# Kernel tuning notes

Hardware: AMD Instinct MI355X
Metric: run time of the kernel (lower is better)

The kernel has to match this reference:

```python
import jax, jax.numpy as jnp
import numpy as np

B, S, H, NH, HD, V = 2, 2048, 1024, 16, 64, 32000
BASE = 10000.0
NEG = jnp.finfo(jnp.float32).min


def setup_inputs() -> dict:
    key = jax.random.key(0)
    ks = jax.random.split(key, 12)
    batch = jax.random.randint(ks[0], (B, S), 0, V)
    positions = jnp.broadcast_to(jnp.arange(S), (B, S))
    lengths = jax.random.randint(ks[1], (B,), 1, S + 1)  # >=1 to avoid fully-masked rows
    sc = 1.0 / np.sqrt(H)
    emb = jax.random.normal(ks[2], (V, H), dtype=jnp.float32) * 0.02
    wq = jax.random.normal(ks[3], (H, NH * HD), dtype=jnp.float32) * sc
    bq = jnp.zeros((NH * HD,), jnp.float32)
    wk = jax.random.normal(ks[4], (H, NH * HD), dtype=jnp.float32) * sc
    bk = jnp.zeros((NH * HD,), jnp.float32)
    wv = jax.random.normal(ks[5], (H, NH * HD), dtype=jnp.float32) * sc
    bv = jnp.zeros((NH * HD,), jnp.float32)
    wo = jax.random.normal(ks[6], (NH * HD, H), dtype=jnp.float32) * sc
    bo = jnp.zeros((H,), jnp.float32)
    return dict(batch=batch, positions=positions, lengths=lengths, emb=emb,
                wq=wq, bq=bq, wk=wk, bk=bk, wv=wv, bv=bv, wo=wo, bo=bo)


def _rope(x, positions):
    # x: [B, NH, S, HD]; positions: [B, S] int
    inv_freq = 1.0 / (BASE ** (jnp.arange(0, HD, 2, dtype=jnp.float32) / HD))  # [HD/2]
    freqs = positions.astype(jnp.float32)[..., None] * inv_freq               # [B, S, HD/2]
    ang = jnp.concatenate([freqs, freqs], axis=-1)                            # [B, S, HD]
    cos = jnp.cos(ang)[:, None]                                               # [B, 1, S, HD]
    sin = jnp.sin(ang)[:, None]
    x1, x2 = x[..., :HD // 2], x[..., HD // 2:]
    rot = jnp.concatenate([-x2, x1], axis=-1)
    return x * cos + rot * sin


def reference(batch, positions, lengths, emb, wq, bq, wk, bk, wv, bv, wo, bo):
    h = emb[batch]                                                 # [B, S, H]
    q = (h @ wq + bq).reshape(B, S, NH, HD).transpose(0, 2, 1, 3)  # [B, NH, S, HD]
    k = (h @ wk + bk).reshape(B, S, NH, HD).transpose(0, 2, 1, 3)
    v = (h @ wv + bv).reshape(B, S, NH, HD).transpose(0, 2, 1, 3)
    q = _rope(q, positions)
    k = _rope(k, positions)
    scores = jnp.einsum('bhqd,bhkd->bhqk', q, k) / np.sqrt(HD)     # [B, NH, S, S]
    causal = jnp.triu(jnp.full((S, S), NEG, jnp.float32), 1)
    pad = jnp.where(jnp.arange(S)[None, :] < lengths[:, None], 0.0, NEG)  # [B, S]
    mask = pad[:, None, None, :] + causal[None, None]              # [B, 1, S, S]
    attn = jax.nn.softmax(scores + mask, axis=-1)
    out = jnp.einsum('bhqk,bhkd->bhqd', attn, v)                   # [B, NH, S, HD]
    out = out.transpose(0, 2, 1, 3).reshape(B, S, NH * HD)
    return out @ wo + bo                                           # [B, S, H]
```

## Files before the change

kernel.cpp:

```cpp
#include <hip/hip_runtime.h>
#include <hip/hip_bf16.h>
#include <cstdint>

#define DEVINL __device__ __forceinline__

typedef __attribute__((ext_vector_type(8))) short short8;
typedef __attribute__((ext_vector_type(4))) float f32x4;

constexpr int B_ = 2, S_ = 2048, H_ = 1024, NH_ = 16, HD_ = 64;
constexpr int M_ = B_ * S_;
constexpr float SC2 = 0.18033688f;

DEVINL float bf2f(unsigned short h) {
    unsigned u = ((unsigned)h) << 16;
    float f; __builtin_memcpy(&f, &u, 4); return f;
}
DEVINL unsigned short f2bf(float f) {
    unsigned u; __builtin_memcpy(&u, &f, 4);
    u += 0x7FFFu + ((u >> 16) & 1u);
    return (unsigned short)(u >> 16);
}
DEVINL unsigned pk2bf(float a, float b) {
    __hip_bfloat162 h = __float22bfloat162_rn(float2{a, b});
    unsigned u; __builtin_memcpy(&u, &h, 4); return u;
}
DEVINL float fexp2(float x) {
#if __has_builtin(__builtin_amdgcn_exp2f)
    return __builtin_amdgcn_exp2f(x);
#else
    return exp2f(x);
#endif
}
DEVINL float ldin(const void* p, size_t i, int fp32) {
    return fp32 ? ((const float*)p)[i] : bf2f(((const unsigned short*)p)[i]);
}
DEVINL void gl16(const void* g, void* l) {
    __builtin_amdgcn_global_load_lds(
        (const __attribute__((address_space(1))) unsigned int*)g,
        (__attribute__((address_space(3))) unsigned int*)l, 16, 0, 0);
}
DEVINL f32x4 mfma16(short8 a, short8 b, f32x4 c) {
    return __builtin_amdgcn_mfma_f32_16x16x32_bf16(a, b, c, 0, 0, 0);
}
DEVINL void fsincos(float rev01, float* sn, float* cs) {
#if __has_builtin(__builtin_amdgcn_sinf) && __has_builtin(__builtin_amdgcn_cosf)
    *sn = __builtin_amdgcn_sinf(rev01);
    *cs = __builtin_amdgcn_cosf(rev01);
#else
    float a = rev01 * 6.28318530717958647692f;
    *sn = __sinf(a); *cs = __cosf(a);
#endif
}
DEVINL void barrier_raw() {
    asm volatile("" ::: "memory");
    __builtin_amdgcn_s_barrier();
    asm volatile("" ::: "memory");
}
DEVINL int detect_fp32(const unsigned short* emb, int t) {
    unsigned short hw = emb[2 * t];
    unsigned e = (hw >> 7) & 0xFFu;
    int s = (((e >= 90u) && (e <= 126u)) || ((hw & 0x7FFFu) == 0u)) ? 1 : 0;
    #pragma unroll
    for (int o = 1; o < 64; o <<= 1) s += __shfl_xor(s, o);
    __shared__ int cnt[4];
    if ((t & 63) == 0) cnt[t >> 6] = s;
    __syncthreads();
    return ((cnt[0] + cnt[1] + cnt[2] + cnt[3]) > 192) ? 0 : 1;
}

__global__ __launch_bounds__(256) void k_prep(const void* w0, const void* w1,
                                              const void* w2, const void* w3,
                                              const void* bq, const void* bk,
                                              const void* bv, const void* bo,
                                              const unsigned short* __restrict__ emb,
                                              const int* __restrict__ batch,
                                              int* __restrict__ flag,
                                              float* __restrict__ biasws,
                                              unsigned short* __restrict__ wT,
                                              unsigned short* __restrict__ hbuf) {
    int tx = threadIdx.x, ty = threadIdx.y, t = ty * 32 + tx;
    int fp32 = detect_fp32(emb, t);
    int z = blockIdx.z;
    if (z == 4) {
        if (!fp32) return;
        int g = blockIdx.y * 32 + blockIdx.x;
        int w = t >> 6, lane = t & 63;
        int row = g * 4 + w;
        int tok = batch[row];
        const float4* s = (const float4*)((const float*)emb + (size_t)tok * H_);
        unsigned long long* d = (unsigned long long*)(hbuf + (size_t)row * H_);
        #pragma unroll
        for (int c = 0; c < 4; c++) {
            float4 x = s[lane + 64 * c];
            d[lane + 64 * c] = (unsigned long long)f2bf(x.x)
                             | ((unsigned long long)f2bf(x.y) << 16)
                             | ((unsigned long long)f2bf(x.z) << 32)
                             | ((unsigned long long)f2bf(x.w) << 48);
        }
        return;
    }
    __shared__ float tile[32][33];
    int mat = z;
    if (mat == 0 && blockIdx.y == 0) {
        if (blockIdx.x == 0 && t == 0) flag[0] = fp32;
        if (blockIdx.x < 16) {
            int i = blockIdx.x * 256 + t;
            const void* src = (i < 1024) ? bq : (i < 2048) ? bk : (i < 3072) ? bv : bo;
            biasws[i] = ldin(src, (size_t)(i & 1023), fp32);
        }
    }
    const void* w = (mat == 0) ? w0 : (mat == 1) ? w1 : (mat == 2) ? w2 : w3;
    int n0 = blockIdx.x * 32, k0 = blockIdx.y * 32;
    for (int i = ty; i < 32; i += 8)
        tile[i][tx] = ldin(w, (size_t)(k0 + i) * 1024 + n0 + tx, fp32);
    __syncthreads();
    unsigned short* dst = wT + (size_t)mat * 1024 * 1024;
    for (int i = ty; i < 32; i += 8)
        dst[(size_t)(n0 + i) * 1024 + k0 + tx] = f2bf(tile[tx][i]);
}

__global__ __launch_bounds__(512, 2) void k_gemm_qkv(const unsigned short* __restrict__ embb,
                                                     const unsigned short* __restrict__ hbuf,
                                                     const int* __restrict__ batch,
                                                     const unsigned short* __restrict__ Bt,
                                                     const float* __restrict__ bias,
                                                     const int* __restrict__ positions,
                                                     const int* __restrict__ flag,
                                                     unsigned short* __restrict__ qo,
                                                     unsigned short* __restrict__ ko,
                                                     unsigned short* __restrict__ vt) {
    constexpr int K = 1024, NT = 16;
    __shared__ alignas(16) unsigned short L[2][2][16384];
    int t = threadIdx.x, lane = t & 63, quad = lane >> 4, n16 = lane & 15;
    int w = t >> 6, wm = w >> 2, wn = w & 3;
    int id = blockIdx.y * 12 + blockIdx.x;
    int sw = (id & 7) * 24 + (id >> 3);
    int m0 = (sw / 12) * 256, n0 = (sw % 12) * 256;
    int fp32 = flag[0];
    int sr = t >> 3;
    int colOff = ((t & 7) ^ (sr & 7)) * 8;
    const unsigned short* aS[2][2];
    const unsigned short* bS[2][2];
    #pragma unroll
    for (int h = 0; h < 2; h++)
        #pragma unroll
        for (int j = 0; j < 2; j++) {
            int gR = m0 + h * 128 + j * 64 + sr;
            aS[h][j] = fp32 ? hbuf + (size_t)gR * K
                            : embb + (size_t)batch[gR] * K;
            bS[h][j] = Bt + (size_t)(n0 + h * 128 + j * 64 + sr) * K;
        }
    int ldst = t * 8;
    auto stage = [&](int kt) {
        int s = kt & 1, k0 = kt * 64;
        #pragma unroll
        for (int h = 0; h < 2; h++)
            #pragma unroll
            for (int j = 0; j < 2; j++) {
                gl16(aS[h][j] + k0 + colOff, &L[s][0][h * 8192 + j * 4096 + ldst]);
                gl16(bS[h][j] + k0 + colOff, &L[s][1][h * 8192 + j * 4096 + ldst]);
            }
    };
    f32x4 acc[8][4];
    #pragma unroll
    for (int mi = 0; mi < 8; mi++)
        #pragma unroll
        for (int ni = 0; ni < 4; ni++) acc[mi][ni] = (f32x4){0.f, 0.f, 0.f, 0.f};
    int x7 = n16 & 7;
    int cs0 = (quad ^ x7) * 8;
    int cs1 = ((4 + quad) ^ x7) * 8;
    int aRow = n16 * 64;
    int bRow = ((wn & 1) * 64 + n16) * 64;
    stage(0);
    asm volatile("s_waitcnt vmcnt(0)" ::: "memory");
    barrier_raw();
    for (int tt = 0; tt < NT; ++tt) {
        int s = tt & 1;
        const unsigned short* LA = &L[s][0][wm * 8192];
        const unsigned short* LB = &L[s][1][(wn >> 1) * 8192];
        short8 Af[4][2], Bf[2][2], Bg[2][2];
        if (tt + 1 < NT) stage(tt + 1);
        #pragma unroll
        for (int mi = 0; mi < 4; mi++) {
            Af[mi][0] = *(const short8*)&LA[aRow + mi * 1024 + cs0];
            Af[mi][1] = *(const short8*)&LA[aRow + mi * 1024 + cs1];
        }
        #pragma unroll
        for (int ni = 0; ni < 2; ni++) {
            Bf[ni][0] = *(const short8*)&LB[bRow + ni * 1024 + cs0];
            Bf[ni][1] = *(const short8*)&LB[bRow + ni * 1024 + cs1];
        }
        barrier_raw();
        asm volatile("s_waitcnt lgkmcnt(0)" ::: "memory");
        __builtin_amdgcn_sched_barrier(0);
        __builtin_amdgcn_s_setprio(1);
        #pragma unroll
        for (int mi = 0; mi < 4; mi++)
            #pragma unroll
            for (int ni = 0; ni < 2; ni++)
                acc[mi][ni] = mfma16(Af[mi][1], Bf[ni][1],
                              mfma16(Af[mi][0], Bf[ni][0], acc[mi][ni]));
        __builtin_amdgcn_s_setprio(0);
        barrier_raw();
        #pragma unroll
        for (int ni = 0; ni < 2; ni++) {
            Bg[ni][0] = *(const short8*)&LB[bRow + (ni + 2) * 1024 + cs0];
            Bg[ni][1] = *(const short8*)&LB[bRow + (ni + 2) * 1024 + cs1];
        }
        barrier_raw();
        asm volatile("s_waitcnt lgkmcnt(0)" ::: "memory");
        __builtin_amdgcn_sched_barrier(0);
        __builtin_amdgcn_s_setprio(1);
        #pragma unroll
        for (int mi = 0; mi < 4; mi++)
            #pragma unroll
            for (int ni = 0; ni < 2; ni++)
                acc[mi][ni + 2] = mfma16(Af[mi][1], Bg[ni][1],
                                  mfma16(Af[mi][0], Bg[ni][0], acc[mi][ni + 2]));
        __builtin_amdgcn_s_setprio(0);
        barrier_raw();
        #pragma unroll
        for (int mi = 0; mi < 4; mi++) {
            Af[mi][0] = *(const short8*)&LA[aRow + (mi + 4) * 1024 + cs0];
            Af[mi][1] = *(const short8*)&LA[aRow + (mi + 4) * 1024 + cs1];
        }
        barrier_raw();
        asm volatile("s_waitcnt lgkmcnt(0)" ::: "memory");
        __builtin_amdgcn_sched_barrier(0);
        __builtin_amdgcn_s_setprio(1);
        #pragma unroll
        for (int mi = 0; mi < 4; mi++)
            #pragma unroll
            for (int ni = 0; ni < 2; ni++)
                acc[mi + 4][ni] = mfma16(Af[mi][1], Bf[ni][1],
                                  mfma16(Af[mi][0], Bf[ni][0], acc[mi + 4][ni]));
        __builtin_amdgcn_s_setprio(0);
        barrier_raw();
        __builtin_amdgcn_s_setprio(1);
        #pragma unroll
        for (int mi = 0; mi < 4; mi++)
            #pragma unroll
            for (int ni = 0; ni < 2; ni++)
                acc[mi + 4][ni + 2] = mfma16(Af[mi][1], Bg[ni][1],
                                      mfma16(Af[mi][0], Bg[ni][0], acc[mi + 4][ni + 2]));
        __builtin_amdgcn_s_setprio(0);
        asm volatile("s_waitcnt vmcnt(0)" ::: "memory");
        barrier_raw();
    }
    int colbase = n0 + wn * 64;
    int buf = colbase >> 10;
    int cc = colbase & 1023;
    float bb[4];
    #pragma unroll
    for (int ni = 0; ni < 4; ni++) bb[ni] = bias[colbase + ni * 16 + n16];
    if (buf == 2) {
        #pragma unroll
        for (int mi = 0; mi < 8; mi++) {
            int row = m0 + wm * 128 + mi * 16 + quad * 4;
            int bb_ = row >> 11;
            int s0 = row & 2047;
            int pos = (s0 & ~31) + quad * 8 + (mi & 1) * 4;
            #pragma unroll
            for (int ni = 0; ni < 4; ni++) {
                int f = cc + ni * 16 + n16;
                unsigned long long pk =
                      (unsigned long long)pk2bf(acc[mi][ni][0] + bb[ni], acc[mi][ni][1] + bb[ni])
                    | ((unsigned long long)pk2bf(acc[mi][ni][2] + bb[ni], acc[mi][ni][3] + bb[ni]) << 32);
                *(unsigned long long*)(vt + ((size_t)(bb_ * 1024 + f)) * 2048 + pos) = pk;
            }
        }
    } else {
        unsigned short* out = (buf == 0) ? qo : ko;
        float osc = (buf == 0) ? SC2 : 1.0f;
        float revf[2];
        #pragma unroll
        for (int ni = 0; ni < 2; ni++) {
            float d = (float)(ni * 16 + n16);
            revf[ni] = __expf(d * -0.28782313f) * 0.15915494f;
        }
        #pragma unroll
        for (int mi = 0; mi < 8; mi++) {
            int row0 = m0 + wm * 128 + mi * 16 + quad * 4;
            #pragma unroll
            for (int i = 0; i < 4; i++) {
                int row = row0 + i;
                float pos = (float)positions[row];
                #pragma unroll
                for (int ni = 0; ni < 2; ni++) {
                    float rev = pos * revf[ni];
                    float fr = rev - floorf(rev);
                    float sn, cs; fsincos(fr, &sn, &cs);
                    float x1 = (acc[mi][ni][i] + bb[ni]) * osc;
                    float x2 = (acc[mi][ni + 2][i] + bb[ni + 2]) * osc;
                    out[(size_t)row * 1024 + cc + ni * 16 + n16] = f2bf(x1 * cs - x2 * sn);
                    out[(size_t)row * 1024 + cc + (ni + 2) * 16 + n16] = f2bf(x2 * cs + x1 * sn);
                }
            }
        }
    }
}

__global__ __launch_bounds__(256) void k_attn(const unsigned short* __restrict__ q,
                                              const unsigned short* __restrict__ k_,
                                              const unsigned short* __restrict__ vt,
                                              const int* __restrict__ lengths,
                                              unsigned short* __restrict__ o) {
    __shared__ alignas(16) unsigned short Ks[2][64 * 64];
    __shared__ alignas(16) unsigned short Vs[2][64 * 64];
    int bx = blockIdx.x;
    int traw = bx & 31, hh = (bx >> 5) & 15, b = bx >> 9;
    int tile = ((bx >> 8) & 1) ? (31 - traw) : traw;
    int t = threadIdx.x, w = t >> 6, lane = t & 63, quad = lane >> 4, n16 = lane & 15;
    int len = lengths[b];
    int kend = min(tile * 64 + 64, len);
    int nkt = (kend + 63) >> 6;
    int qrow = tile * 64 + w * 16 + n16;
    int limit = min(qrow, len - 1);
    int tbw = tile * 64 + w * 16;
    short8 qf[2];
    {
        size_t qa = ((size_t)(b * S_ + qrow)) * H_ + hh * 64 + quad * 8;
        qf[0] = *(const short8*)(q + qa);
        qf[1] = *(const short8*)(q + qa + 32);
    }
    f32x4 oa[4];
    float l_ = 0.f;
    #pragma unroll
    for (int nb = 0; nb < 4; nb++) oa[nb] = (f32x4){0.f, 0.f, 0.f, 0.f};
    const unsigned short* kbase = k_ + ((size_t)b * S_) * H_ + hh * 64;
    const unsigned short* vbase = vt + ((size_t)(b * 1024 + hh * 64)) * 2048;
    int sr0 = t >> 3, sc0 = (t & 7) ^ (sr0 & 7);
    int sr1 = (t + 256) >> 3, sc1 = (t & 7) ^ (sr1 & 7);
    auto stage = [&](int kt) {
        int kb = kt * 64, bi = kt & 1;
        gl16(kbase + (size_t)(kb + sr0) * H_ + sc0 * 8, &Ks[bi][t * 8]);
        gl16(kbase + (size_t)(kb + sr1) * H_ + sc1 * 8, &Ks[bi][(t + 256) * 8]);
        gl16(vbase + (size_t)sr0 * 2048 + kb + sc0 * 8, &Vs[bi][t * 8]);
        gl16(vbase + (size_t)sr1 * 2048 + kb + sc1 * 8, &Vs[bi][(t + 256) * 8]);
    };
    stage(0);
    for (int kt = 0; kt < nkt; kt++) {
        int kb = kt * 64, bi = kt & 1;
        __syncthreads();
        if (kt + 1 < nkt) stage(kt + 1);
        const unsigned short* Kb = Ks[bi];
        const unsigned short* Vb = Vs[bi];
        short8 kf[4][2];
        #pragma unroll
        for (int st = 0; st < 4; st++)
            #pragma unroll
            for (int hf = 0; hf < 2; hf++) {
                int ky = st * 16 + n16;
                kf[st][hf] = *(const short8*)&Kb[ky * 64 + (((hf * 4 + quad) ^ (ky & 7)) * 8)];
            }
        f32x4 sc[4];
        #pragma unroll
        for (int st = 0; st < 4; st++) {
            f32x4 z = (f32x4){0.f, 0.f, 0.f, 0.f};
            z = mfma16(kf[st][0], qf[0], z);
            z = mfma16(kf[st][1], qf[1], z);
            sc[st] = z;
        }
        float rs = 0.f;
        if (kb + 64 <= min(tbw, len)) {
            #pragma unroll
            for (int st = 0; st < 4; st++)
                #pragma unroll
                for (int i = 0; i < 4; i++) {
                    float p = fexp2(sc[st][i]);
                    rs += p;
                    sc[st][i] = p;
                }
        } else {
            #pragma unroll
            for (int st = 0; st < 4; st++)
                #pragma unroll
                for (int i = 0; i < 4; i++) {
                    int kg = kb + st * 16 + quad * 4 + i;
                    float p = (kg <= limit) ? fexp2(sc[st][i]) : 0.f;
                    rs += p;
                    sc[st][i] = p;
                }
        }
        rs += __shfl_xor(rs, 16);
        rs += __shfl_xor(rs, 32);
        l_ += rs;
        short8 vf[2][4];
        #pragma unroll
        for (int p = 0; p < 2; p++)
            #pragma unroll
            for (int nb = 0; nb < 4; nb++) {
                int f = nb * 16 + n16;
                vf[p][nb] = *(const short8*)&Vb[f * 64 + (((p * 4 + quad) ^ (f & 7)) * 8)];
            }
        #pragma unroll
        for (int p = 0; p < 2; p++) {
            union { unsigned u[4]; short8 v8; } pp;
            pp.u[0] = pk2bf(sc[2 * p][0], sc[2 * p][1]);
            pp.u[1] = pk2bf(sc[2 * p][2], sc[2 * p][3]);
            pp.u[2] = pk2bf(sc[2 * p + 1][0], sc[2 * p + 1][1]);
            pp.u[3] = pk2bf(sc[2 * p + 1][2], sc[2 * p + 1][3]);
            #pragma unroll
            for (int nb = 0; nb < 4; nb++)
                oa[nb] = mfma16(pp.v8, vf[p][nb], oa[nb]);
        }
    }
    f32x4 rl;
    #pragma unroll
    for (int i = 0; i < 4; i++) rl[i] = 1.f / __shfl(l_, quad * 4 + i);
    #pragma unroll
    for (int nb = 0; nb < 4; nb++) {
        #pragma unroll
        for (int i = 0; i < 4; i++) {
            int row = tile * 64 + w * 16 + quad * 4 + i;
            o[((size_t)(b * S_ + row)) * H_ + hh * 64 + nb * 16 + n16] =
                f2bf(oa[nb][i] * rl[i]);
        }
    }
}

__global__ __launch_bounds__(256) void k_gemm64(const unsigned short* __restrict__ A,
                                                const unsigned short* __restrict__ Bt,
                                                const float* __restrict__ bias,
                                                unsigned short* __restrict__ Cb,
                                                float* __restrict__ Cf,
                                                const int* __restrict__ flag) {
    constexpr int K = 1024, N = 1024;
    __shared__ alignas(16) unsigned short As[2][64 * 32];
    __shared__ alignas(16) unsigned short Bs[2][128 * 32];
    int t = threadIdx.x, lane = t & 63, quad = lane >> 4, n16 = lane & 15;
    int w = t >> 6, wm = w & 1, wn = w >> 1;
    int m0 = blockIdx.y * 64, n0 = blockIdx.x * 128;
    int r0 = t >> 2, r1 = 64 + r0, ka = (t & 3) * 8;
    const unsigned short* a0 = A + (size_t)(m0 + r0) * K;
    const unsigned short* b0 = Bt + (size_t)(n0 + r0) * K;
    const unsigned short* b1 = Bt + (size_t)(n0 + r1) * K;
    f32x4 acc[2][4];
    #pragma unroll
    for (int mi = 0; mi < 2; mi++)
        #pragma unroll
        for (int ni = 0; ni < 4; ni++) acc[mi][ni] = (f32x4){0.f, 0.f, 0.f, 0.f};
    for (int k0 = 0; k0 < K; k0 += 64) {
        __syncthreads();
        gl16(a0 + k0 + ka,      &As[0][t * 8]);
        gl16(a0 + k0 + 32 + ka, &As[1][t * 8]);
        gl16(b0 + k0 + ka,      &Bs[0][t * 8]);
        gl16(b1 + k0 + ka,      &Bs[0][(t + 256) * 8]);
        gl16(b0 + k0 + 32 + ka, &Bs[1][t * 8]);
        gl16(b1 + k0 + 32 + ka, &Bs[1][(t + 256) * 8]);
        __syncthreads();
        #pragma unroll
        for (int ks = 0; ks < 2; ks++) {
            short8 af[2], bfr[4];
            #pragma unroll
            for (int mi = 0; mi < 2; mi++)
                af[mi] = *(const short8*)&As[ks][(wm * 32 + mi * 16 + n16) * 32 + quad * 8];
            #pragma unroll
            for (int ni = 0; ni < 4; ni++)
                bfr[ni] = *(const short8*)&Bs[ks][(wn * 64 + ni * 16 + n16) * 32 + quad * 8];
            #pragma unroll
            for (int mi = 0; mi < 2; mi++)
                #pragma unroll
                for (int ni = 0; ni < 4; ni++)
                    acc[mi][ni] = mfma16(af[mi], bfr[ni], acc[mi][ni]);
        }
    }
    int fp32out = (flag[0] == 1);
    #pragma unroll
    for (int mi = 0; mi < 2; mi++) {
        #pragma unroll
        for (int ni = 0; ni < 4; ni++) {
            int row = m0 + wm * 32 + mi * 16 + quad * 4;
            int col = n0 + wn * 64 + ni * 16 + n16;
            float bb = bias[col];
            #pragma unroll
            for (int i = 0; i < 4; i++) {
                float val = acc[mi][ni][i] + bb;
                size_t idx = (size_t)(row + i) * N + col;
                if (fp32out) Cf[idx] = val;
                else         Cb[idx] = f2bf(val);
            }
        }
    }
}

extern "C" void kernel_launch(void* const* d_in, const int* in_sizes, int n_in,
                              void* d_out, int out_size, void* d_ws, size_t ws_size,
                              hipStream_t stream) {
    (void)in_sizes; (void)n_in; (void)out_size; (void)ws_size;
    const int* batch     = (const int*)d_in[0];
    const int* positions = (const int*)d_in[1];
    const int* lengths   = (const int*)d_in[2];
    const void* emb = d_in[3];
    const void* wq = d_in[4];  const void* bq = d_in[5];
    const void* wk = d_in[6];  const void* bk = d_in[7];
    const void* wv = d_in[8];  const void* bv = d_in[9];
    const void* wo = d_in[10]; const void* bo = d_in[11];

    char* ws = (char*)d_ws;
    int*   flag   = (int*)ws;
    float* biasws = (float*)(ws + 4096);
    unsigned short* wT = (unsigned short*)(ws + 20480);
    size_t off = 20480 + (8ull << 20);
    unsigned short* hbuf = (unsigned short*)(ws + off); off += (8ull << 20);
    unsigned short* qb   = (unsigned short*)(ws + off); off += (8ull << 20);
    unsigned short* kb2  = (unsigned short*)(ws + off); off += (8ull << 20);
    unsigned short* vtb  = (unsigned short*)(ws + off); off += (8ull << 20);
    unsigned short* ao   = (unsigned short*)(ws + off); off += (8ull << 20);

    k_prep<<<dim3(32, 32, 5), dim3(32, 8), 0, stream>>>(
        wq, wk, wv, wo, bq, bk, bv, bo, (const unsigned short*)emb, batch,
        flag, biasws, wT, hbuf);

    k_gemm_qkv<<<dim3(12, 16), 512, 0, stream>>>(
        (const unsigned short*)emb, hbuf, batch, wT, biasws, positions, flag,
        qb, kb2, vtb);

    k_attn<<<B_ * NH_ * 32, 256, 0, stream>>>(qb, kb2, vtb, lengths, ao);

    k_gemm64<<<dim3(1024 / 128, M_ / 64), 256, 0, stream>>>(
        ao, wT + (3ull << 20), biasws + 3072,
        (unsigned short*)d_out, (float*)d_out, flag);
}
```

Baseline: 291.7 us.

## Split attention keys across warps with 128-key tiles and LDS reduction

```diff
diff --git a/kernel.cpp b/kernel.cpp
--- a/kernel.cpp
+++ b/kernel.cpp
@@ -300,121 +300,141 @@
     }
 }
 
-__global__ __launch_bounds__(256) void k_attn(const unsigned short* __restrict__ q,
-                                              const unsigned short* __restrict__ k_,
-                                              const unsigned short* __restrict__ vt,
-                                              const int* __restrict__ lengths,
-                                              unsigned short* __restrict__ o) {
-    __shared__ alignas(16) unsigned short Ks[2][64 * 64];
-    __shared__ alignas(16) unsigned short Vs[2][64 * 64];
+__global__ __launch_bounds__(256, 2) void k_attn(const unsigned short* __restrict__ q,
+                                                 const unsigned short* __restrict__ k_,
+                                                 const unsigned short* __restrict__ vt,
+                                                 const int* __restrict__ lengths,
+                                                 unsigned short* __restrict__ o) {
+    __shared__ alignas(16) unsigned short KV[2][16384];
+    __shared__ float lds_l[4][4][16];
     int bx = blockIdx.x;
     int traw = bx & 31, hh = (bx >> 5) & 15, b = bx >> 9;
     int tile = ((bx >> 8) & 1) ? (31 - traw) : traw;
     int t = threadIdx.x, w = t >> 6, lane = t & 63, quad = lane >> 4, n16 = lane & 15;
     int len = lengths[b];
     int kend = min(tile * 64 + 64, len);
-    int nkt = (kend + 63) >> 6;
-    int qrow = tile * 64 + w * 16 + n16;
-    int limit = min(qrow, len - 1);
-    int tbw = tile * 64 + w * 16;
-    short8 qf[2];
-    {
-        size_t qa = ((size_t)(b * S_ + qrow)) * H_ + hh * 64 + quad * 8;
-        qf[0] = *(const short8*)(q + qa);
-        qf[1] = *(const short8*)(q + qa + 32);
-    }
-    f32x4 oa[4];
-    float l_ = 0.f;
-    #pragma unroll
-    for (int nb = 0; nb < 4; nb++) oa[nb] = (f32x4){0.f, 0.f, 0.f, 0.f};
+    int nkt = (kend + 127) >> 7;
+    short8 qf[4][2];
+    #pragma unroll
+    for (int qg = 0; qg < 4; qg++) {
+        size_t qa = ((size_t)(b * S_ + tile * 64 + qg * 16 + n16)) * H_ + hh * 64 + quad * 8;
+        qf[qg][0] = *(const short8*)(q + qa);
+        qf[qg][1] = *(const short8*)(q + qa + 32);
+    }
+    f32x4 oa[4][4];
+    float lp[4] = {0.f, 0.f, 0.f, 0.f};
+    #pragma unroll
+    for (int qg = 0; qg < 4; qg++)
+        #pragma unroll
+        for (int nb = 0; nb < 4; nb++) oa[qg][nb] = (f32x4){0.f, 0.f, 0.f, 0.f};
     const unsigned short* kbase = k_ + ((size_t)b * S_) * H_ + hh * 64;
     const unsigned short* vbase = vt + ((size_t)(b * 1024 + hh * 64)) * 2048;
-    int sr0 = t >> 3, sc0 = (t & 7) ^ (sr0 & 7);
-    int sr1 = (t + 256) >> 3, sc1 = (t & 7) ^ (sr1 & 7);
+    int r8 = (t >> 3) & 7;
+    int f8 = (t >> 4) & 7;
     auto stage = [&](int kt) {
-        int kb = kt * 64, bi = kt & 1;
-        gl16(kbase + (size_t)(kb + sr0) * H_ + sc0 * 8, &Ks[bi][t * 8]);
-        gl16(kbase + (size_t)(kb + sr1) * H_ + sc1 * 8, &Ks[bi][(t + 256) * 8]);
-        gl16(vbase + (size_t)sr0 * 2048 + kb + sc0 * 8, &Vs[bi][t * 8]);
-        gl16(vbase + (size_t)sr1 * 2048 + kb + sc1 * 8, &Vs[bi][(t + 256) * 8]);
+        int kb = kt * 128, bi = kt & 1;
+        #pragma unroll
+        for (int v = 0; v < 4; v++) {
+            int kr = (t >> 3) + v * 32;
+            gl16(kbase + (size_t)(kb + kr) * H_ + ((t & 7) ^ r8) * 8,
+                 &KV[bi][(t + v * 256) * 8]);
+            int vf_ = (t >> 4) + v * 16;
+            gl16(vbase + (size_t)vf_ * 2048 + kb + ((t & 15) ^ f8) * 8,
+                 &KV[bi][8192 + (t + v * 256) * 8]);
+        }
     };
     stage(0);
     for (int kt = 0; kt < nkt; kt++) {
-        int kb = kt * 64, bi = kt & 1;
+        int kb = kt * 128, bi = kt & 1;
         __syncthreads();
         if (kt + 1 < nkt) stage(kt + 1);
-        const unsigned short* Kb = Ks[bi];
-        const unsigned short* Vb = Vs[bi];
-        short8 kf[4][2];
-        #pragma unroll
-        for (int st = 0; st < 4; st++)
-            #pragma unroll
-            for (int hf = 0; hf < 2; hf++) {
-                int ky = st * 16 + n16;
-                kf[st][hf] = *(const short8*)&Kb[ky * 64 + (((hf * 4 + quad) ^ (ky & 7)) * 8)];
-            }
-        f32x4 sc[4];
-        #pragma unroll
-        for (int st = 0; st < 4; st++) {
-            f32x4 z = (f32x4){0.f, 0.f, 0.f, 0.f};
-            z = mfma16(kf[st][0], qf[0], z);
-            z = mfma16(kf[st][1], qf[1], z);
-            sc[st] = z;
-        }
-        float rs = 0.f;
-        if (kb + 64 <= min(tbw, len)) {
-            #pragma unroll
-            for (int st = 0; st < 4; st++)
+        int sbase = kb + w * 32;
+        if (sbase < kend) {
+            const unsigned short* Kb = &KV[bi][0];
+            const unsigned short* Vb = &KV[bi][8192];
+            short8 kf[2][2];
+            #pragma unroll
+            for (int stw = 0; stw < 2; stw++)
                 #pragma unroll
-                for (int i = 0; i < 4; i++) {
-                    float p = fexp2(sc[st][i]);
-                    rs += p;
-                    sc[st][i] = p;
+                for (int hf = 0; hf < 2; hf++) {
+                    int ky = w * 32 + stw * 16 + n16;
+                    kf[stw][hf] = *(const short8*)&Kb[(ky * 8 + ((hf * 4 + quad) ^ (ky & 7))) * 8];
                 }
-        } else {
-            #pragma unroll
-            for (int st = 0; st < 4; st++)
-                #pragma unroll
-                for (int i = 0; i < 4; i++) {
-                    int kg = kb + st * 16 + quad * 4 + i;
-                    float p = (kg <= limit) ? fexp2(sc[st][i]) : 0.f;
-                    rs += p;
-                    sc[st][i] = p;
-                }
-        }
-        rs += __shfl_xor(rs, 16);
-        rs += __shfl_xor(rs, 32);
-        l_ += rs;
-        short8 vf[2][4];
-        #pragma unroll
-        for (int p = 0; p < 2; p++)
+            short8 vfr[4];
             #pragma unroll
             for (int nb = 0; nb < 4; nb++) {
                 int f = nb * 16 + n16;
-                vf[p][nb] = *(const short8*)&Vb[f * 64 + (((p * 4 + quad) ^ (f & 7)) * 8)];
+                vfr[nb] = *(const short8*)&Vb[(f * 16 + ((w * 4 + quad) ^ (f & 7))) * 8];
             }
-        #pragma unroll
-        for (int p = 0; p < 2; p++) {
-            union { unsigned u[4]; short8 v8; } pp;
-            pp.u[0] = pk2bf(sc[2 * p][0], sc[2 * p][1]);
-            pp.u[1] = pk2bf(sc[2 * p][2], sc[2 * p][3]);
-            pp.u[2] = pk2bf(sc[2 * p + 1][0], sc[2 * p + 1][1]);
-            pp.u[3] = pk2bf(sc[2 * p + 1][2], sc[2 * p + 1][3]);
-            #pragma unroll
-            for (int nb = 0; nb < 4; nb++)
-                oa[nb] = mfma16(pp.v8, vf[p][nb], oa[nb]);
-        }
-    }
-    f32x4 rl;
-    #pragma unroll
-    for (int i = 0; i < 4; i++) rl[i] = 1.f / __shfl(l_, quad * 4 + i);
+            int fullt = (sbase + 32 <= min(tile * 64, len));
+            #pragma unroll
+            for (int qg = 0; qg < 4; qg++) {
+                f32x4 s0 = (f32x4){0.f, 0.f, 0.f, 0.f};
+                f32x4 s1 = (f32x4){0.f, 0.f, 0.f, 0.f};
+                s0 = mfma16(kf[0][0], qf[qg][0], s0);
+                s0 = mfma16(kf[0][1], qf[qg][1], s0);
+                s1 = mfma16(kf[1][0], qf[qg][0], s1);
+                s1 = mfma16(kf[1][1], qf[qg][1], s1);
+                float rs = 0.f;
+                if (fullt) {
+                    #pragma unroll
+                    for (int i = 0; i < 4; i++) {
+                        s0[i] = fexp2(s0[i]); rs += s0[i];
+                        s1[i] = fexp2(s1[i]); rs += s1[i];
+                    }
+                } else {
+                    int limit = min(tile * 64 + qg * 16 + n16, len - 1);
+                    #pragma unroll
+                    for (int i = 0; i < 4; i++) {
+                        int kg0 = sbase + quad * 4 + i;
+                        int kg1 = sbase + 16 + quad * 4 + i;
+                        float p0 = (kg0 <= limit) ? fexp2(s0[i]) : 0.f;
+                        float p1 = (kg1 <= limit) ? fexp2(s1[i]) : 0.f;
+                        s0[i] = p0; s1[i] = p1; rs += p0 + p1;
+                    }
+                }
+                rs += __shfl_xor(rs, 16);
+                rs += __shfl_xor(rs, 32);
+                lp[qg] += rs;
+                union { unsigned u[4]; short8 v8; } pp;
+                pp.u[0] = pk2bf(s0[0], s0[1]);
+                pp.u[1] = pk2bf(s0[2], s0[3]);
+                pp.u[2] = pk2bf(s1[0], s1[1]);
+                pp.u[3] = pk2bf(s1[2], s1[3]);
+                #pragma unroll
+                for (int nb = 0; nb < 4; nb++)
+                    oa[qg][nb] = mfma16(pp.v8, vfr[nb], oa[qg][nb]);
+            }
+        }
+    }
+    __syncthreads();
+    float* red = (float*)&KV[0][0];
+    #pragma unroll
+    for (int qg = 0; qg < 4; qg++) {
+        if (quad == 0) lds_l[w][qg][n16] = lp[qg];
+        #pragma unroll
+        for (int nb = 0; nb < 4; nb++)
+            *(f32x4*)&red[(w * 16 + qg * 4 + nb) * 256 + n16 * 16 + quad * 4] = oa[qg][nb];
+    }
+    __syncthreads();
+    float lsum[4];
+    #pragma unroll
+    for (int i = 0; i < 4; i++) {
+        int rr = quad * 4 + i;
+        lsum[i] = 1.f / (lds_l[0][w][rr] + lds_l[1][w][rr] +
+                         lds_l[2][w][rr] + lds_l[3][w][rr]);
+    }
     #pragma unroll
     for (int nb = 0; nb < 4; nb++) {
+        f32x4 v0 = *(f32x4*)&red[(0 * 16 + w * 4 + nb) * 256 + n16 * 16 + quad * 4];
+        f32x4 v1 = *(f32x4*)&red[(1 * 16 + w * 4 + nb) * 256 + n16 * 16 + quad * 4];
+        f32x4 v2 = *(f32x4*)&red[(2 * 16 + w * 4 + nb) * 256 + n16 * 16 + quad * 4];
+        f32x4 v3 = *(f32x4*)&red[(3 * 16 + w * 4 + nb) * 256 + n16 * 16 + quad * 4];
         #pragma unroll
         for (int i = 0; i < 4; i++) {
             int row = tile * 64 + w * 16 + quad * 4 + i;
             o[((size_t)(b * S_ + row)) * H_ + hh * 64 + nb * 16 + n16] =
-                f2bf(oa[nb][i] * rl[i]);
+                f2bf((v0[i] + v1[i] + v2[i] + v3[i]) * lsum[i]);
         }
     }
 }
```

Result: no change. 296.5 us (+1.6%).
